# Kernel tuning notes

Hardware: AMD Instinct MI355X
Metric: run time of the kernel (lower is better)

The kernel has to match this reference:

```python
import jax, jax.numpy as jnp
import numpy as np

N_NODES = 100000
N_EDGES = 1600000
NUM_FEATURES = 128


def setup_inputs() -> dict:
    key = jax.random.key(0)
    ks = jax.random.split(key, 10)
    x = jax.random.normal(ks[0], (N_NODES, NUM_FEATURES), dtype=jnp.float32)
    edge_index = jax.random.randint(ks[1], (2, N_EDGES), 0, N_NODES, dtype=jnp.int64)
    # conv1 MLP: Linear(num_features,128) -> ReLU -> Linear(128,128)
    s1 = 1.0 / np.sqrt(NUM_FEATURES)
    W1 = jax.random.uniform(ks[2], (NUM_FEATURES, 128), jnp.float32, -s1, s1)
    b1 = jax.random.uniform(ks[3], (128,), jnp.float32, -s1, s1)
    s2 = 1.0 / np.sqrt(128)
    W2 = jax.random.uniform(ks[4], (128, 128), jnp.float32, -s2, s2)
    b2 = jax.random.uniform(ks[5], (128,), jnp.float32, -s2, s2)
    # conv2 MLP: Linear(128,64) -> ReLU -> Linear(64,64)
    W3 = jax.random.uniform(ks[6], (128, 64), jnp.float32, -s2, s2)
    b3 = jax.random.uniform(ks[7], (64,), jnp.float32, -s2, s2)
    s3 = 1.0 / np.sqrt(64)
    W4 = jax.random.uniform(ks[8], (64, 64), jnp.float32, -s3, s3)
    b4 = jax.random.uniform(ks[9], (64,), jnp.float32, -s3, s3)
    return {"x": x, "edge_index": edge_index, "W1": W1, "b1": b1,
            "W2": W2, "b2": b2, "W3": W3, "b3": b3, "W4": W4, "b4": b4}


def _gin_conv(x, src, dst, Wa, ba, Wb, bb):
    # GINConv with eps=0: out = MLP(x + sum_{j->i} x_j)
    agg = jax.ops.segment_sum(x[src], dst, num_segments=N_NODES)
    h = x + agg
    h = jax.nn.relu(h @ Wa + ba)
    return h @ Wb + bb


def reference(x, edge_index, W1, b1, W2, b2, W3, b3, W4, b4):
    src, dst = edge_index[0], edge_index[1]
    h = jax.nn.relu(_gin_conv(x, src, dst, W1, b1, W2, b2))
    h = jax.nn.relu(_gin_conv(h, src, dst, W3, b3, W4, b4))
    return h
```

## Files before the change

### kernel.cpp

```cpp
#include <hip/hip_runtime.h>
#include <hip/hip_bf16.h>

#define NODES 100000
#define EDGES 1600000
#define NBINS ((NODES + 255) >> 8)
#define BINCAP 8192
#define PB_BLOCKS 128
#define PB_CHUNK ((EDGES + PB_BLOCKS - 1) / PB_BLOCKS)
#define CAST_BLOCKS 12500

typedef __bf16 bf16x8 __attribute__((ext_vector_type(8)));
typedef float f32x4 __attribute__((ext_vector_type(4)));

__device__ __forceinline__ unsigned short f2b(float f) {
  __hip_bfloat16 h = __float2bfloat16(f);
  return __builtin_bit_cast(unsigned short, h);
}
__device__ __forceinline__ float b_lo(unsigned u) { return __uint_as_float(u << 16); }
__device__ __forceinline__ float b_hi(unsigned u) { return __uint_as_float(u & 0xffff0000u); }

__global__ __launch_bounds__(256) void prep_all(
    const float4* __restrict__ x4, ushort4* __restrict__ xh4,
    const float* __restrict__ W1, const float* __restrict__ W2,
    const float* __restrict__ W3, const float* __restrict__ W4,
    unsigned short* __restrict__ Wt1, unsigned short* __restrict__ Wt2,
    unsigned short* __restrict__ Wt3, unsigned short* __restrict__ Wt4) {
  const int b = blockIdx.x;
  if (b < CAST_BLOCKS) {
    int i = b * 256 + threadIdx.x;
    float4 v = x4[i];
    ushort4 o;
    o.x = f2b(v.x); o.y = f2b(v.y); o.z = f2b(v.z); o.w = f2b(v.w);
    xh4[i] = o;
    return;
  }
  int i = (b - CAST_BLOCKS) * 256 + threadIdx.x;
  if (i < 16384) {
    int n = i >> 7, k = i & 127;
    Wt1[i] = f2b(W1[k * 128 + n]);
  } else if (i < 32768) {
    int j = i - 16384; int n = j >> 7, k = j & 127;
    Wt2[j] = f2b(W2[k * 128 + n]);
  } else if (i < 40960) {
    int j = i - 32768; int n = j >> 7, k = j & 127;
    Wt3[j] = f2b(W3[k * 64 + n]);
  } else if (i < 45056) {
    int j = i - 40960; int n = j >> 6, k = j & 63;
    Wt4[j] = f2b(W4[k * 64 + n]);
  }
}

__global__ __launch_bounds__(256) void bin_count(const int* __restrict__ dst,
                                                 int* __restrict__ partial) {
  __shared__ int h[NBINS];
  for (int i = threadIdx.x; i < NBINS; i += 256) h[i] = 0;
  __syncthreads();
  const int beg = blockIdx.x * PB_CHUNK;
  const int end = min(beg + PB_CHUNK, EDGES);
  for (int e = beg + threadIdx.x; e < end; e += 256)
    atomicAdd(&h[dst[e] >> 8], 1);
  __syncthreads();
  for (int i = threadIdx.x; i < NBINS; i += 256)
    partial[blockIdx.x * NBINS + i] = h[i];
}

__global__ __launch_bounds__(512) void scan_bins(const int* __restrict__ partial,
                                                 int* __restrict__ binStart,
                                                 int* __restrict__ blockoff,
                                                 int* __restrict__ rowstart) {
  __shared__ int s[512];
  const int t = threadIdx.x;
  int v = 0;
  if (t < NBINS)
    for (int b = 0; b < PB_BLOCKS; b++) v += partial[b * NBINS + t];
  s[t] = v;
  __syncthreads();
  for (int off = 1; off < 512; off <<= 1) {
    int u = (t >= off) ? s[t - off] : 0;
    __syncthreads();
    s[t] += u;
    __syncthreads();
  }
  if (t < NBINS) binStart[t] = s[t] - v;
  if (t == 0) {
    binStart[NBINS] = EDGES;
    rowstart[NODES] = EDGES;
  }
  if (t < NBINS) {
    int run = 0;
    for (int b = 0; b < PB_BLOCKS; b++) {
      blockoff[b * NBINS + t] = run;
      run += partial[b * NBINS + t];
    }
  }
}

__global__ __launch_bounds__(256) void bin_scatter(const int* __restrict__ src,
                                                   const int* __restrict__ dst,
                                                   const int* __restrict__ binStart,
                                                   const int* __restrict__ blockoff,
                                                   unsigned* __restrict__ coarse) {
  __shared__ int base[NBINS];
  __shared__ int h[NBINS];
  const int beg = blockIdx.x * PB_CHUNK;
  const int end = min(beg + PB_CHUNK, EDGES);
  for (int i = threadIdx.x; i < NBINS; i += 256) {
    base[i] = binStart[i] + blockoff[blockIdx.x * NBINS + i];
    h[i] = 0;
  }
  __syncthreads();
  for (int e = beg + threadIdx.x; e < end; e += 256) {
    int d = dst[e];
    int b = d >> 8;
    int pos = base[b] + atomicAdd(&h[b], 1);
    coarse[pos] = (unsigned)src[e] | ((unsigned)(d & 255) << 17);
  }
}

__global__ __launch_bounds__(256) void bin_fine(const unsigned* __restrict__ coarse,
                                                const int* __restrict__ binStart,
                                                int* __restrict__ rowstart,
                                                int* __restrict__ bucket) {
  __shared__ unsigned ent[BINCAP];
  __shared__ unsigned obuf[BINCAP];
  __shared__ int deg[256];
  __shared__ int pre[256];
  const int b = blockIdx.x;
  const int t = threadIdx.x;
  const int s0 = binStart[b];
  const int nE = binStart[b + 1] - s0;
  const int binBase = b << 8;

  deg[t] = 0;
  __syncthreads();
  for (int i = t; i < nE; i += 256) {
    unsigned e = coarse[s0 + i];
    ent[i] = e;
    atomicAdd(&deg[e >> 17], 1);
  }
  __syncthreads();
  int v = deg[t];
  pre[t] = v;
  __syncthreads();
  for (int off = 1; off < 256; off <<= 1) {
    int u = (t >= off) ? pre[t - off] : 0;
    __syncthreads();
    pre[t] += u;
    __syncthreads();
  }
  int ex = pre[t] - v;
  if (binBase + t < NODES) rowstart[binBase + t] = s0 + ex;
  deg[t] = ex;
  __syncthreads();
  for (int i = t; i < nE; i += 256) {
    unsigned e = ent[i];
    int pos = atomicAdd(&deg[e >> 17], 1);
    obuf[pos] = e & 0x1FFFFu;
  }
  __syncthreads();
  for (int i = t; i < nE; i += 256) bucket[s0 + i] = (int)obuf[i];
}

__global__ __launch_bounds__(256) void gather_sum_bf16(
    const uint4* __restrict__ xq, const int* __restrict__ rowstart,
    const int* __restrict__ bucket, uint4* __restrict__ outq) {
  const int n = blockIdx.x * 4 + (threadIdx.x >> 6);
  if (n >= NODES) return;
  const int lane = threadIdx.x & 63;
  const int g = lane >> 4;
  const int fl = lane & 15;

  float a[8] = {0.f, 0.f, 0.f, 0.f, 0.f, 0.f, 0.f, 0.f};
  if (g == 0) {
    uint4 v = xq[(size_t)n * 16 + fl];
    a[0] = b_lo(v.x); a[1] = b_hi(v.x);
    a[2] = b_lo(v.y); a[3] = b_hi(v.y);
    a[4] = b_lo(v.z); a[5] = b_hi(v.z);
    a[6] = b_lo(v.w); a[7] = b_hi(v.w);
  }

  const int beg = rowstart[n];
  const int end = rowstart[n + 1];
  for (int j = beg; j < end; j += 8) {
    int e0 = j + g;
    int e1 = j + 4 + g;
    int i0 = (e0 < end) ? e0 : (end - 1);
    int i1 = (e1 < end) ? e1 : (end - 1);
    int s0 = bucket[i0];
    int s1 = bucket[i1];
    uint4 v0 = xq[(size_t)s0 * 16 + fl];
    uint4 v1 = xq[(size_t)s1 * 16 + fl];
    float m0 = (e0 < end) ? 1.f : 0.f;
    float m1 = (e1 < end) ? 1.f : 0.f;
    a[0] = fmaf(b_lo(v0.x), m0, a[0]); a[1] = fmaf(b_hi(v0.x), m0, a[1]);
    a[2] = fmaf(b_lo(v0.y), m0, a[2]); a[3] = fmaf(b_hi(v0.y), m0, a[3]);
    a[4] = fmaf(b_lo(v0.z), m0, a[4]); a[5] = fmaf(b_hi(v0.z), m0, a[5]);
    a[6] = fmaf(b_lo(v0.w), m0, a[6]); a[7] = fmaf(b_hi(v0.w), m0, a[7]);
    a[0] = fmaf(b_lo(v1.x), m1, a[0]); a[1] = fmaf(b_hi(v1.x), m1, a[1]);
    a[2] = fmaf(b_lo(v1.y), m1, a[2]); a[3] = fmaf(b_hi(v1.y), m1, a[3]);
    a[4] = fmaf(b_lo(v1.z), m1, a[4]); a[5] = fmaf(b_hi(v1.z), m1, a[5]);
    a[6] = fmaf(b_lo(v1.w), m1, a[6]); a[7] = fmaf(b_hi(v1.w), m1, a[7]);
  }

#pragma unroll
  for (int k = 0; k < 8; k++) {
    a[k] += __shfl_xor(a[k], 16, 64);
    a[k] += __shfl_xor(a[k], 32, 64);
  }

  if (lane < 16) {
    uint4 o;
    o.x = ((unsigned)f2b(a[1]) << 16) | f2b(a[0]);
    o.y = ((unsigned)f2b(a[3]) << 16) | f2b(a[2]);
    o.z = ((unsigned)f2b(a[5]) << 16) | f2b(a[4]);
    o.w = ((unsigned)f2b(a[7]) << 16) | f2b(a[6]);
    outq[(size_t)n * 16 + fl] = o;
  }
}

template <int K, int N1, int N2, bool OUT_F32>
__global__ __launch_bounds__(256, 4) void mlp_fused(
    const unsigned short* __restrict__ A,
    const unsigned short* __restrict__ Wa, const float* __restrict__ ba,
    const unsigned short* __restrict__ Wb, const float* __restrict__ bb,
    void* __restrict__ Cout, int M) {
  constexpr int LDA = K + 8;
  constexpr int NT1 = N1 / 16, KB1 = K / 32;
  constexpr int NT2 = N2 / 16, KB2 = N1 / 32;
  constexpr int NMAX = (N1 > N2 ? N1 : N2);
  __shared__ unsigned short S[64 * LDA];
  __shared__ unsigned short Wbuf[2][NMAX * 32];

  const int tid = threadIdx.x;
  const int wave = tid >> 6;
  const int lane = tid & 63;
  const int g = lane >> 4;
  const int fl = lane & 15;
  const int rowBase = blockIdx.x * 64;

  for (int i = tid; i < 64 * (K / 8); i += 256) {
    int r = i / (K / 8), c = i % (K / 8);
    uint4 v = make_uint4(0, 0, 0, 0);
    if (rowBase + r < M)
      v = ((const uint4*)A)[(size_t)(rowBase + r) * (K / 8) + c];
    *(uint4*)&S[r * LDA + c * 8] = v;
  }
  for (int i = tid; i < N1 * 4; i += 256) {
    int n = i >> 2, c = i & 3;
    *(uint4*)&Wbuf[0][n * 32 + c * 8] = *(const uint4*)&Wa[(size_t)n * K + c * 8];
  }
  __syncthreads();

  const int arow = wave * 16 + fl;

  f32x4 acc[NT1];
#pragma unroll
  for (int c = 0; c < NT1; c++) acc[c] = (f32x4){0.f, 0.f, 0.f, 0.f};
#pragma unroll
  for (int kb = 0; kb < KB1; kb++) {
    if (kb + 1 < KB1) {
      for (int i = tid; i < N1 * 4; i += 256) {
        int n = i >> 2, c = i & 3;
        *(uint4*)&Wbuf[(kb + 1) & 1][n * 32 + c * 8] =
            *(const uint4*)&Wa[(size_t)n * K + (kb + 1) * 32 + c * 8];
      }
    }
    bf16x8 av = *(const bf16x8*)&S[arow * LDA + kb * 32 + g * 8];
#pragma unroll
    for (int c = 0; c < NT1; c++) {
      bf16x8 bv = *(const bf16x8*)&Wbuf[kb & 1][(c * 16 + fl) * 32 + g * 8];
      acc[c] = __builtin_amdgcn_mfma_f32_16x16x32_bf16(av, bv, acc[c], 0, 0, 0);
    }
    __syncthreads();
  }

#pragma unroll
  for (int c = 0; c < NT1; c++) {
    int col = c * 16 + fl;
    float bv = ba[col];
#pragma unroll
    for (int reg = 0; reg < 4; reg++) {
      int rloc = wave * 16 + g * 4 + reg;
      S[rloc * LDA + col] = f2b(fmaxf(acc[c][reg] + bv, 0.f));
    }
  }

  for (int i = tid; i < N2 * 4; i += 256) {
    int n = i >> 2, c = i & 3;
    *(uint4*)&Wbuf[0][n * 32 + c * 8] = *(const uint4*)&Wb[(size_t)n * N1 + c * 8];
  }
  __syncthreads();

  f32x4 acc2[NT2];
#pragma unroll
  for (int c = 0; c < NT2; c++) acc2[c] = (f32x4){0.f, 0.f, 0.f, 0.f};
#pragma unroll
  for (int kb = 0; kb < KB2; kb++) {
    if (kb + 1 < KB2) {
      for (int i = tid; i < N2 * 4; i += 256) {
        int n = i >> 2, c = i & 3;
        *(uint4*)&Wbuf[(kb + 1) & 1][n * 32 + c * 8] =
            *(const uint4*)&Wb[(size_t)n * N1 + (kb + 1) * 32 + c * 8];
      }
    }
    bf16x8 av = *(const bf16x8*)&S[arow * LDA + kb * 32 + g * 8];
#pragma unroll
    for (int c = 0; c < NT2; c++) {
      bf16x8 bv = *(const bf16x8*)&Wbuf[kb & 1][(c * 16 + fl) * 32 + g * 8];
      acc2[c] = __builtin_amdgcn_mfma_f32_16x16x32_bf16(av, bv, acc2[c], 0, 0, 0);
    }
    __syncthreads();
  }

#pragma unroll
  for (int c = 0; c < NT2; c++) {
    int col = c * 16 + fl;
    float bv = bb[col];
#pragma unroll
    for (int reg = 0; reg < 4; reg++) {
      int row = rowBase + wave * 16 + g * 4 + reg;
      if (row < M) {
        float v = fmaxf(acc2[c][reg] + bv, 0.f);
        if (OUT_F32)
          ((float*)Cout)[(size_t)row * N2 + col] = v;
        else
          ((unsigned short*)Cout)[(size_t)row * N2 + col] = f2b(v);
      }
    }
  }
}

extern "C" void kernel_launch(void* const* d_in, const int* in_sizes, int n_in,
                              void* d_out, int out_size, void* d_ws, size_t ws_size,
                              hipStream_t stream) {
  const float* x = (const float*)d_in[0];
  const int* ei = (const int*)d_in[1];
  const int* src = ei;
  const int* dst = ei + EDGES;
  const float* W1 = (const float*)d_in[2];
  const float* b1 = (const float*)d_in[3];
  const float* W2 = (const float*)d_in[4];
  const float* b2 = (const float*)d_in[5];
  const float* W3 = (const float*)d_in[6];
  const float* b3 = (const float*)d_in[7];
  const float* W4 = (const float*)d_in[8];
  const float* b4 = (const float*)d_in[9];
  float* out = (float*)d_out;

  char* ws = (char*)d_ws;
  unsigned short* xh = (unsigned short*)ws;
  unsigned short* hA = xh + (size_t)NODES * 128;
  unsigned short* hB = hA + (size_t)NODES * 128;
  unsigned short* Wt1 = hB + (size_t)NODES * 128;
  unsigned short* Wt2 = Wt1 + 128 * 128;
  unsigned short* Wt3 = Wt2 + 128 * 128;
  unsigned short* Wt4 = Wt3 + 64 * 128;
  int* rowstart = (int*)(Wt4 + 64 * 64);
  int* binStart = rowstart + NODES + 1;
  int* partial = binStart + NBINS + 1;
  int* blockoff = partial + PB_BLOCKS * NBINS;
  unsigned* coarse = (unsigned*)(blockoff + PB_BLOCKS * NBINS);
  int* bucket = (int*)(coarse + EDGES);

  const int nblocks4 = (NODES + 3) / 4;
  const int gblocks = (NODES + 63) / 64;

  prep_all<<<CAST_BLOCKS + 176, 256, 0, stream>>>(
      (const float4*)x, (ushort4*)xh, W1, W2, W3, W4, Wt1, Wt2, Wt3, Wt4);
  bin_count<<<PB_BLOCKS, 256, 0, stream>>>(dst, partial);
  scan_bins<<<1, 512, 0, stream>>>(partial, binStart, blockoff, rowstart);
  bin_scatter<<<PB_BLOCKS, 256, 0, stream>>>(src, dst, binStart, blockoff, coarse);
  bin_fine<<<NBINS, 256, 0, stream>>>(coarse, binStart, rowstart, bucket);

  gather_sum_bf16<<<nblocks4, 256, 0, stream>>>((const uint4*)xh, rowstart, bucket,
                                                (uint4*)hA);
  mlp_fused<128, 128, 128, false><<<gblocks, 256, 0, stream>>>(
      hA, Wt1, b1, Wt2, b2, hB, NODES);

  gather_sum_bf16<<<nblocks4, 256, 0, stream>>>((const uint4*)hB, rowstart, bucket,
                                                (uint4*)hA);
  mlp_fused<128, 64, 64, true><<<gblocks, 256, 0, stream>>>(
      hA, Wt3, b3, Wt4, b4, out, NODES);
}
```

Baseline: 357.6 us.

## Fuse bin counting into prep kernel, parallelize block-offset scan, unroll gather

The edge bin-count pass is merged into the x/weight cast kernel so both run in one launch. The old single-block scan, which looped serially over 128 partial counts per bin, is split into a per-bin parallel scan over a transposed partial array plus a small totals scan. The gather loop now handles 16 edges per iteration instead of 8, putting more loads in flight. The costs are one extra launch, higher register pressure in the gather, and more wasted masked loads on low-degree nodes.

```diff
diff --git a/kernel.cpp b/kernel.cpp
--- a/kernel.cpp
+++ b/kernel.cpp
@@ -8,6 +8,7 @@
 #define PB_BLOCKS 128
 #define PB_CHUNK ((EDGES + PB_BLOCKS - 1) / PB_BLOCKS)
 #define CAST_BLOCKS 12500
+#define WPREP_BLOCKS 176
 
 typedef __bf16 bf16x8 __attribute__((ext_vector_type(8)));
 typedef float f32x4 __attribute__((ext_vector_type(4)));
@@ -19,12 +20,14 @@
 __device__ __forceinline__ float b_lo(unsigned u) { return __uint_as_float(u << 16); }
 __device__ __forceinline__ float b_hi(unsigned u) { return __uint_as_float(u & 0xffff0000u); }
 
-__global__ __launch_bounds__(256) void prep_all(
+__global__ __launch_bounds__(256) void prep_count(
     const float4* __restrict__ x4, ushort4* __restrict__ xh4,
     const float* __restrict__ W1, const float* __restrict__ W2,
     const float* __restrict__ W3, const float* __restrict__ W4,
     unsigned short* __restrict__ Wt1, unsigned short* __restrict__ Wt2,
-    unsigned short* __restrict__ Wt3, unsigned short* __restrict__ Wt4) {
+    unsigned short* __restrict__ Wt3, unsigned short* __restrict__ Wt4,
+    const int* __restrict__ dst, int* __restrict__ partialT) {
+  __shared__ int h[NBINS];
   const int b = blockIdx.x;
   if (b < CAST_BLOCKS) {
     int i = b * 256 + threadIdx.x;
@@ -34,45 +37,60 @@
     xh4[i] = o;
     return;
   }
-  int i = (b - CAST_BLOCKS) * 256 + threadIdx.x;
-  if (i < 16384) {
-    int n = i >> 7, k = i & 127;
-    Wt1[i] = f2b(W1[k * 128 + n]);
-  } else if (i < 32768) {
-    int j = i - 16384; int n = j >> 7, k = j & 127;
-    Wt2[j] = f2b(W2[k * 128 + n]);
-  } else if (i < 40960) {
-    int j = i - 32768; int n = j >> 7, k = j & 127;
-    Wt3[j] = f2b(W3[k * 64 + n]);
-  } else if (i < 45056) {
-    int j = i - 40960; int n = j >> 6, k = j & 63;
-    Wt4[j] = f2b(W4[k * 64 + n]);
-  }
-}
-
-__global__ __launch_bounds__(256) void bin_count(const int* __restrict__ dst,
-                                                 int* __restrict__ partial) {
-  __shared__ int h[NBINS];
+  if (b < CAST_BLOCKS + WPREP_BLOCKS) {
+    int i = (b - CAST_BLOCKS) * 256 + threadIdx.x;
+    if (i < 16384) {
+      int n = i >> 7, k = i & 127;
+      Wt1[i] = f2b(W1[k * 128 + n]);
+    } else if (i < 32768) {
+      int j = i - 16384; int n = j >> 7, k = j & 127;
+      Wt2[j] = f2b(W2[k * 128 + n]);
+    } else if (i < 40960) {
+      int j = i - 32768; int n = j >> 7, k = j & 127;
+      Wt3[j] = f2b(W3[k * 64 + n]);
+    } else if (i < 45056) {
+      int j = i - 40960; int n = j >> 6, k = j & 63;
+      Wt4[j] = f2b(W4[k * 64 + n]);
+    }
+    return;
+  }
+  const int cb = b - CAST_BLOCKS - WPREP_BLOCKS;
   for (int i = threadIdx.x; i < NBINS; i += 256) h[i] = 0;
   __syncthreads();
-  const int beg = blockIdx.x * PB_CHUNK;
+  const int beg = cb * PB_CHUNK;
   const int end = min(beg + PB_CHUNK, EDGES);
   for (int e = beg + threadIdx.x; e < end; e += 256)
     atomicAdd(&h[dst[e] >> 8], 1);
   __syncthreads();
   for (int i = threadIdx.x; i < NBINS; i += 256)
-    partial[blockIdx.x * NBINS + i] = h[i];
-}
-
-__global__ __launch_bounds__(512) void scan_bins(const int* __restrict__ partial,
-                                                 int* __restrict__ binStart,
-                                                 int* __restrict__ blockoff,
-                                                 int* __restrict__ rowstart) {
+    partialT[i * PB_BLOCKS + cb] = h[i];
+}
+
+__global__ __launch_bounds__(128) void scan_blockoff(const int* __restrict__ partialT,
+                                                     int* __restrict__ blockoffT,
+                                                     int* __restrict__ binTotal) {
+  __shared__ int s[128];
+  const int bin = blockIdx.x;
+  const int t = threadIdx.x;
+  int v = partialT[bin * PB_BLOCKS + t];
+  s[t] = v;
+  __syncthreads();
+  for (int off = 1; off < 128; off <<= 1) {
+    int u = (t >= off) ? s[t - off] : 0;
+    __syncthreads();
+    s[t] += u;
+    __syncthreads();
+  }
+  blockoffT[bin * PB_BLOCKS + t] = s[t] - v;
+  if (t == 127) binTotal[bin] = s[127];
+}
+
+__global__ __launch_bounds__(512) void scan_totals(const int* __restrict__ binTotal,
+                                                   int* __restrict__ binStart,
+                                                   int* __restrict__ rowstart) {
   __shared__ int s[512];
   const int t = threadIdx.x;
-  int v = 0;
-  if (t < NBINS)
-    for (int b = 0; b < PB_BLOCKS; b++) v += partial[b * NBINS + t];
+  int v = (t < NBINS) ? binTotal[t] : 0;
   s[t] = v;
   __syncthreads();
   for (int off = 1; off < 512; off <<= 1) {
@@ -86,26 +104,19 @@
     binStart[NBINS] = EDGES;
     rowstart[NODES] = EDGES;
   }
-  if (t < NBINS) {
-    int run = 0;
-    for (int b = 0; b < PB_BLOCKS; b++) {
-      blockoff[b * NBINS + t] = run;
-      run += partial[b * NBINS + t];
-    }
-  }
 }
 
 __global__ __launch_bounds__(256) void bin_scatter(const int* __restrict__ src,
                                                    const int* __restrict__ dst,
                                                    const int* __restrict__ binStart,
-                                                   const int* __restrict__ blockoff,
+                                                   const int* __restrict__ blockoffT,
                                                    unsigned* __restrict__ coarse) {
   __shared__ int base[NBINS];
   __shared__ int h[NBINS];
   const int beg = blockIdx.x * PB_CHUNK;
   const int end = min(beg + PB_CHUNK, EDGES);
   for (int i = threadIdx.x; i < NBINS; i += 256) {
-    base[i] = binStart[i] + blockoff[blockIdx.x * NBINS + i];
+    base[i] = binStart[i] + blockoffT[i * PB_BLOCKS + blockIdx.x];
     h[i] = 0;
   }
   __syncthreads();
@@ -181,17 +192,21 @@
 
   const int beg = rowstart[n];
   const int end = rowstart[n + 1];
-  for (int j = beg; j < end; j += 8) {
-    int e0 = j + g;
-    int e1 = j + 4 + g;
+  for (int j = beg; j < end; j += 16) {
+    int e0 = j + g, e1 = j + 4 + g, e2 = j + 8 + g, e3 = j + 12 + g;
     int i0 = (e0 < end) ? e0 : (end - 1);
     int i1 = (e1 < end) ? e1 : (end - 1);
-    int s0 = bucket[i0];
-    int s1 = bucket[i1];
+    int i2 = (e2 < end) ? e2 : (end - 1);
+    int i3 = (e3 < end) ? e3 : (end - 1);
+    int s0 = bucket[i0], s1 = bucket[i1], s2 = bucket[i2], s3 = bucket[i3];
     uint4 v0 = xq[(size_t)s0 * 16 + fl];
     uint4 v1 = xq[(size_t)s1 * 16 + fl];
+    uint4 v2 = xq[(size_t)s2 * 16 + fl];
+    uint4 v3 = xq[(size_t)s3 * 16 + fl];
     float m0 = (e0 < end) ? 1.f : 0.f;
     float m1 = (e1 < end) ? 1.f : 0.f;
+    float m2 = (e2 < end) ? 1.f : 0.f;
+    float m3 = (e3 < end) ? 1.f : 0.f;
     a[0] = fmaf(b_lo(v0.x), m0, a[0]); a[1] = fmaf(b_hi(v0.x), m0, a[1]);
     a[2] = fmaf(b_lo(v0.y), m0, a[2]); a[3] = fmaf(b_hi(v0.y), m0, a[3]);
     a[4] = fmaf(b_lo(v0.z), m0, a[4]); a[5] = fmaf(b_hi(v0.z), m0, a[5]);
@@ -200,6 +215,14 @@
     a[2] = fmaf(b_lo(v1.y), m1, a[2]); a[3] = fmaf(b_hi(v1.y), m1, a[3]);
     a[4] = fmaf(b_lo(v1.z), m1, a[4]); a[5] = fmaf(b_hi(v1.z), m1, a[5]);
     a[6] = fmaf(b_lo(v1.w), m1, a[6]); a[7] = fmaf(b_hi(v1.w), m1, a[7]);
+    a[0] = fmaf(b_lo(v2.x), m2, a[0]); a[1] = fmaf(b_hi(v2.x), m2, a[1]);
+    a[2] = fmaf(b_lo(v2.y), m2, a[2]); a[3] = fmaf(b_hi(v2.y), m2, a[3]);
+    a[4] = fmaf(b_lo(v2.z), m2, a[4]); a[5] = fmaf(b_hi(v2.z), m2, a[5]);
+    a[6] = fmaf(b_lo(v2.w), m2, a[6]); a[7] = fmaf(b_hi(v2.w), m2, a[7]);
+    a[0] = fmaf(b_lo(v3.x), m3, a[0]); a[1] = fmaf(b_hi(v3.x), m3, a[1]);
+    a[2] = fmaf(b_lo(v3.y), m3, a[2]); a[3] = fmaf(b_hi(v3.y), m3, a[3]);
+    a[4] = fmaf(b_lo(v3.z), m3, a[4]); a[5] = fmaf(b_hi(v3.z), m3, a[5]);
+    a[6] = fmaf(b_lo(v3.w), m3, a[6]); a[7] = fmaf(b_hi(v3.w), m3, a[7]);
   }
 
 #pragma unroll
@@ -357,19 +380,21 @@
   unsigned short* Wt4 = Wt3 + 64 * 128;
   int* rowstart = (int*)(Wt4 + 64 * 64);
   int* binStart = rowstart + NODES + 1;
-  int* partial = binStart + NBINS + 1;
-  int* blockoff = partial + PB_BLOCKS * NBINS;
-  unsigned* coarse = (unsigned*)(blockoff + PB_BLOCKS * NBINS);
+  int* binTotal = binStart + NBINS + 1;
+  int* partialT = binTotal + NBINS;
+  int* blockoffT = partialT + NBINS * PB_BLOCKS;
+  unsigned* coarse = (unsigned*)(blockoffT + NBINS * PB_BLOCKS);
   int* bucket = (int*)(coarse + EDGES);
 
   const int nblocks4 = (NODES + 3) / 4;
   const int gblocks = (NODES + 63) / 64;
 
-  prep_all<<<CAST_BLOCKS + 176, 256, 0, stream>>>(
-      (const float4*)x, (ushort4*)xh, W1, W2, W3, W4, Wt1, Wt2, Wt3, Wt4);
-  bin_count<<<PB_BLOCKS, 256, 0, stream>>>(dst, partial);
-  scan_bins<<<1, 512, 0, stream>>>(partial, binStart, blockoff, rowstart);
-  bin_scatter<<<PB_BLOCKS, 256, 0, stream>>>(src, dst, binStart, blockoff, coarse);
+  prep_count<<<CAST_BLOCKS + WPREP_BLOCKS + PB_BLOCKS, 256, 0, stream>>>(
+      (const float4*)x, (ushort4*)xh, W1, W2, W3, W4, Wt1, Wt2, Wt3, Wt4,
+      dst, partialT);
+  scan_blockoff<<<NBINS, 128, 0, stream>>>(partialT, blockoffT, binTotal);
+  scan_totals<<<1, 512, 0, stream>>>(binTotal, binStart, rowstart);
+  bin_scatter<<<PB_BLOCKS, 256, 0, stream>>>(src, dst, binStart, blockoffT, coarse);
   bin_fine<<<NBINS, 256, 0, stream>>>(coarse, binStart, rowstart, bucket);
 
   gather_sum_bf16<<<nblocks4, 256, 0, stream>>>((const uint4*)xh, rowstart, bucket,
```

Result: faster. 341.5 us (-4.5%).
